# Optimization experiments

Hardware: AMD Instinct MI355X
Metric: run time of the kernel (lower is better)

The kernel has to match this reference:

```python
import jax, jax.numpy as jnp
import numpy as np

N_NODES = 100000
N_EDGES = 1600000
D_IN = 64
D_HID = 64
N_CLS = 4


def setup_inputs() -> dict:
    key = jax.random.key(0)
    ks = jax.random.split(key, 8)
    s = lambda d: 1.0 / np.sqrt(d)
    return {
        "node_features": jax.random.normal(ks[0], (N_NODES, D_IN), jnp.float32),
        "edge_src": jax.random.randint(ks[1], (N_EDGES,), 0, N_NODES, jnp.int32),
        "edge_dst": jax.random.randint(ks[2], (N_EDGES,), 0, N_NODES, jnp.int32),
        "W_self1": jax.random.normal(ks[3], (D_IN, D_HID), jnp.float32) * s(D_IN),
        "b_self1": jnp.zeros((D_HID,), jnp.float32),
        "W_neigh1": jax.random.normal(ks[4], (D_IN, D_HID), jnp.float32) * s(D_IN),
        "W_self2": jax.random.normal(ks[5], (D_HID, N_CLS), jnp.float32) * s(D_HID),
        "b_self2": jnp.zeros((N_CLS,), jnp.float32),
        "W_neigh2": jax.random.normal(ks[6], (D_HID, N_CLS), jnp.float32) * s(D_HID),
    }


def _sage_mean(h, edge_src, edge_dst, W_self, b_self, W_neigh, n_nodes):
    # mean aggregation over in-neighbors: gather src feats, segment-sum by dst
    msg_sum = jax.ops.segment_sum(h[edge_src], edge_dst, num_segments=n_nodes)
    deg = jax.ops.segment_sum(
        jnp.ones_like(edge_dst, dtype=h.dtype), edge_dst, num_segments=n_nodes
    )
    h_neigh = msg_sum / jnp.maximum(deg, 1.0)[:, None]
    # DGL SAGEConv: fc_self (with bias) + fc_neigh (no bias)
    return h @ W_self + b_self + h_neigh @ W_neigh


def reference(node_features, edge_src, edge_dst, W_self1, b_self1, W_neigh1,
              W_self2, b_self2, W_neigh2):
    n = node_features.shape[0]
    h1 = jnp.tanh(_sage_mean(node_features, edge_src, edge_dst,
                             W_self1, b_self1, W_neigh1, n))
    logits = _sage_mean(h1, edge_src, edge_dst, W_self2, b_self2, W_neigh2, n)
    return logits
```

## Files before the change

### kernel.cpp

```cpp
#include <hip/hip_runtime.h>
#include <hip/hip_bf16.h>
#include <stdint.h>

typedef unsigned char  u8;
typedef unsigned short u16;
typedef unsigned int   u32;
typedef __attribute__((ext_vector_type(8))) short bf16x8;
typedef __attribute__((ext_vector_type(2))) float f32x2;
typedef __attribute__((ext_vector_type(4))) float f32x4;
typedef __attribute__((ext_vector_type(4))) int   i32x4;
typedef __attribute__((ext_vector_type(2))) u32   u32x2;
typedef __attribute__((ext_vector_type(4))) u32   u32x4;

#define BKT_SHIFT 9
#define BKT_NODES 512
#define CAP 12288
#define BINBLK 512
#define KEYCAP 3200
#define GEMMBLK 512

__device__ __forceinline__ float bf2f(u16 u) { return __uint_as_float(((u32)u) << 16); }
__device__ __forceinline__ u16 f2bf(float f) {
    u32 u = __float_as_uint(f);
    u += 0x7FFFu + ((u >> 16) & 1u);
    return (u16)(u >> 16);
}
__device__ __forceinline__ int pkbf(float a, float b) {
    return (int)__builtin_amdgcn_perm(__float_as_uint(b), __float_as_uint(a), 0x07060302u);
}
__device__ __forceinline__ u8 f2fp8(float v) {
    int p = __builtin_amdgcn_cvt_pk_fp8_f32(v, v, 0, false);
    return (u8)(p & 0xff);
}


__global__ __launch_bounds__(256) void k_front(const float* __restrict__ X,
                                               const float* __restrict__ Ws,
                                               const float* __restrict__ b1,
                                               const float* __restrict__ Wn,
                                               u16* __restrict__ Zb,
                                               u8* __restrict__ Y,
                                               int n,
                                               const int* __restrict__ src,
                                               const int* __restrict__ dst,
                                               int* __restrict__ offT,
                                               u32* __restrict__ binned,
                                               int E, int chunk, int nb) {
    __shared__ __align__(16) char sm[17024];
    int t = threadIdx.x;

    if ((int)blockIdx.x < BINBLK) {
        u32* keys = (u32*)sm;
        int* h    = (int*)(sm + 12800);
        int* cur  = (int*)(sm + 13600);
        int* ws4  = (int*)(sm + 14400);
        int blk = blockIdx.x;
        int beg = blk * chunk, end = min(beg + chunk, E), m = max(0, end - beg);

        for (int i = t; i < nb; i += 256) h[i] = 0;
        __syncthreads();
        for (int i = beg + t; i < end; i += 256) atomicAdd(&h[dst[i] >> BKT_SHIFT], 1);
        __syncthreads();
        int v = (t < nb) ? h[t] : 0;
        int lane = t & 63, w = t >> 6;
        int incl = v;
#pragma unroll
        for (int o = 1; o < 64; o <<= 1) {
            int x = __shfl_up(incl, o, 64);
            if (lane >= o) incl += x;
        }
        if (lane == 63) ws4[w] = incl;
        __syncthreads();
        if (t == 0) {
            int run = 0;
#pragma unroll
            for (int i = 0; i < 4; i++) { ws4[4 + i] = run; run += ws4[i]; }
        }
        __syncthreads();
        int excl = incl - v + ws4[4 + w];
        int* orow = offT + (size_t)blk * (nb + 1);
        if (t < nb) { cur[t] = excl; orow[t] = excl; }
        if (t == nb - 1) orow[nb] = excl + v;
        __syncthreads();
        for (int i = beg + t; i < end; i += 256) {
            int d = dst[i], bk = d >> BKT_SHIFT;
            int p = atomicAdd(&cur[bk], 1);
            keys[p] = ((u32)src[i] << BKT_SHIFT) | (u32)(d & (BKT_NODES - 1));
        }
        __syncthreads();
        u32* outp = binned + (size_t)blk * chunk;
        for (int i = t; i < m; i += 256) outp[i] = keys[i];
        return;
    }

    u16* wl = (u16*)sm;
    for (int i = t; i < 8192; i += 256) {
        int k = i >> 7, c = i & 127;
        float wv = (c < 64) ? Ws[k * 64 + c] : Wn[k * 64 + (c - 64)];
        wl[k * 132 + c] = f2bf(wv);
    }
    __syncthreads();

    int wid = t >> 6, lane = t & 63;
    int lrow = lane & 15, lquad = lane >> 4;

    bf16x8 bfrag[8][2];
#pragma unroll
    for (int ct = 0; ct < 8; ct++)
#pragma unroll
        for (int kf = 0; kf < 2; kf++)
#pragma unroll
            for (int j = 0; j < 8; j++)
                bfrag[ct][kf][j] = (short)wl[(kf * 32 + lquad * 8 + j) * 132 + ct * 16 + lrow];

    float bias[4];
#pragma unroll
    for (int ct = 0; ct < 4; ct++) bias[ct] = b1[ct * 16 + lrow];

    int tiles = n >> 4;
    int tstride = GEMMBLK * 4;
    for (int tile = (blockIdx.x - BINBLK) * 4 + wid; tile < tiles; tile += tstride) {
        int nb4 = tile << 4;

        const float* xp = X + (size_t)(nb4 + lrow) * 64 + lquad * 8;
        f32x4 x0 = *(const f32x4*)(xp);
        f32x4 x1 = *(const f32x4*)(xp + 4);
        f32x4 x2 = *(const f32x4*)(xp + 32);
        f32x4 x3 = *(const f32x4*)(xp + 36);
        i32x4 p0, p1;
        p0.x = pkbf(x0.x, x0.y); p0.y = pkbf(x0.z, x0.w);
        p0.z = pkbf(x1.x, x1.y); p0.w = pkbf(x1.z, x1.w);
        p1.x = pkbf(x2.x, x2.y); p1.y = pkbf(x2.z, x2.w);
        p1.z = pkbf(x3.x, x3.y); p1.w = pkbf(x3.z, x3.w);
        bf16x8 af0 = __builtin_bit_cast(bf16x8, p0);
        bf16x8 af1 = __builtin_bit_cast(bf16x8, p1);

        f32x4 acc[8];
#pragma unroll
        for (int ct = 0; ct < 8; ct++) {
            f32x4 c = {0.f, 0.f, 0.f, 0.f};
            c = __builtin_amdgcn_mfma_f32_16x16x32_bf16(af0, bfrag[ct][0], c, 0, 0, 0);
            c = __builtin_amdgcn_mfma_f32_16x16x32_bf16(af1, bfrag[ct][1], c, 0, 0, 0);
            acc[ct] = c;
        }

        int rbase = nb4 + lquad * 4;
#pragma unroll
        for (int ct = 0; ct < 4; ct++)
#pragma unroll
            for (int r = 0; r < 4; r++)
                Zb[(size_t)(rbase + r) * 64 + ct * 16 + lrow] = f2bf(acc[ct][r] + bias[ct]);
#pragma unroll
        for (int ct = 0; ct < 4; ct++)
#pragma unroll
            for (int r = 0; r < 4; r++)
                Y[(size_t)(rbase + r) * 64 + ct * 16 + lrow] = f2fp8(acc[ct + 4][r]);
    }
}


__global__ __launch_bounds__(512) void k_csr(const u32* __restrict__ binned,
                                             const int* __restrict__ offT,
                                             int* __restrict__ rpb,
                                             int* __restrict__ rpe,
                                             int* __restrict__ col,
                                             int chunk, int nb, int n) {
    __shared__ __align__(16) u32 ed[CAP];
    __shared__ u32 srt[CAP];
    __shared__ int gst[BINBLK], gln[BINBLK], soff[BINBLK];
    __shared__ int cnt[BKT_NODES];
    __shared__ int wsum[8], woff[8];
    __shared__ int stot;
    int b = blockIdx.x, t = threadIdx.x;
    int lane = t & 63, w = t >> 6;

    {
        const int* row = offT + (size_t)t * (nb + 1);
        int s = row[b], e = row[b + 1];
        gst[t] = t * chunk + s;
        gln[t] = e - s;
    }
    __syncthreads();
    int v = gln[t];
    int incl = v;
#pragma unroll
    for (int o = 1; o < 64; o <<= 1) {
        int x = __shfl_up(incl, o, 64);
        if (lane >= o) incl += x;
    }
    if (lane == 63) wsum[w] = incl;
    __syncthreads();
    if (t == 0) {
        int run = 0;
#pragma unroll
        for (int i = 0; i < 8; i++) { woff[i] = run; run += wsum[i]; }
        stot = run;
    }
    __syncthreads();
    soff[t] = incl - v + woff[w];
    __syncthreads();
    int total = min(stot, CAP);
    for (int k = w; k < BINBLK; k += 8) {
        int g = gst[k], L = gln[k], o = soff[k];
        for (int i = lane; i < L && o + i < CAP; i += 64) ed[o + i] = binned[g + i];
    }
    cnt[t] = 0;
    __syncthreads();
    for (int i = t; i < total; i += 512)
        atomicAdd(&cnt[ed[i] & (BKT_NODES - 1)], 1);
    __syncthreads();
    int v2 = cnt[t];
    int incl2 = v2;
#pragma unroll
    for (int o = 1; o < 64; o <<= 1) {
        int x = __shfl_up(incl2, o, 64);
        if (lane >= o) incl2 += x;
    }
    if (lane == 63) wsum[w] = incl2;
    __syncthreads();
    if (t == 0) {
        int run = 0;
#pragma unroll
        for (int i = 0; i < 8; i++) { woff[i] = run; run += wsum[i]; }
    }
    __syncthreads();
    int excl2 = incl2 - v2 + woff[w];
    int gnode = b * BKT_NODES + t;
    int cb = b * CAP;
    if (gnode < n) { rpb[gnode] = cb + excl2; rpe[gnode] = cb + excl2 + v2; }
    cnt[t] = excl2;
    __syncthreads();
    for (int i = t; i < total; i += 512) {
        u32 e = ed[i];
        int p = atomicAdd(&cnt[e & (BKT_NODES - 1)], 1);
        srt[p] = e >> BKT_SHIFT;
    }
    __syncthreads();
    for (int i = t; i < total; i += 512) col[cb + i] = (int)srt[i];
}


__global__ __launch_bounds__(256) void k_gather1f(const int* __restrict__ rpb,
                                                  const int* __restrict__ rpe,
                                                  const int* __restrict__ col,
                                                  const u16* __restrict__ Zb,
                                                  const u8* __restrict__ Y,
                                                  const float* __restrict__ Ws2,
                                                  const float* __restrict__ b2,
                                                  const float* __restrict__ Wn2,
                                                  float* __restrict__ P,
                                                  u16* __restrict__ Q, int n) {
    __shared__ float wl[64 * 9];
    int t = threadIdx.x;
    for (int i = t; i < 512; i += 256) {
        int k = i >> 3, c = i & 7;
        float v = (c < 4) ? Ws2[k * 4 + c] : Wn2[k * 4 + (c - 4)];
        wl[((k & 7) * 8 + (k >> 3)) * 9 + c] = v;
    }
    float bb0 = b2[0], bb1 = b2[1], bb2 = b2[2], bb3 = b2[3];
    __syncthreads();

    int w = t >> 6;
    int g = (t >> 3) & 7;
    int l8 = t & 7;
    int node = blockIdx.x * 32 + w * 8 + g;
    if (node >= n) return;

    int beg = rpb[node], end = rpe[node];
    float a[8];
#pragma unroll
    for (int j = 0; j < 8; j++) a[j] = 0.f;

    const u8* yb = Y + (size_t)l8 * 8;
    int e = beg;
    for (; e + 4 <= end; e += 4) {
        i32x4 cv = *(const i32x4*)(col + e);
        u32x2 y0 = *(const u32x2*)(yb + (size_t)cv.x * 64);
        u32x2 y1 = *(const u32x2*)(yb + (size_t)cv.y * 64);
        u32x2 y2 = *(const u32x2*)(yb + (size_t)cv.z * 64);
        u32x2 y3 = *(const u32x2*)(yb + (size_t)cv.w * 64);
#pragma unroll
        for (int j = 0; j < 4; j++) {
            u32x2 yw = (j == 0) ? y0 : (j == 1) ? y1 : (j == 2) ? y2 : y3;
            f32x2 lo0 = __builtin_amdgcn_cvt_pk_f32_fp8(yw.x, false);
            f32x2 hi0 = __builtin_amdgcn_cvt_pk_f32_fp8(yw.x, true);
            f32x2 lo1 = __builtin_amdgcn_cvt_pk_f32_fp8(yw.y, false);
            f32x2 hi1 = __builtin_amdgcn_cvt_pk_f32_fp8(yw.y, true);
            a[0] += lo0.x; a[1] += lo0.y; a[2] += hi0.x; a[3] += hi0.y;
            a[4] += lo1.x; a[5] += lo1.y; a[6] += hi1.x; a[7] += hi1.y;
        }
    }
    for (; e < end; e++) {
        u32x2 yw = *(const u32x2*)(yb + (size_t)col[e] * 64);
        f32x2 lo0 = __builtin_amdgcn_cvt_pk_f32_fp8(yw.x, false);
        f32x2 hi0 = __builtin_amdgcn_cvt_pk_f32_fp8(yw.x, true);
        f32x2 lo1 = __builtin_amdgcn_cvt_pk_f32_fp8(yw.y, false);
        f32x2 hi1 = __builtin_amdgcn_cvt_pk_f32_fp8(yw.y, true);
        a[0] += lo0.x; a[1] += lo0.y; a[2] += hi0.x; a[3] += hi0.y;
        a[4] += lo1.x; a[5] += lo1.y; a[6] += hi1.x; a[7] += hi1.y;
    }

    float deg = (float)(end - beg);
    float inv = (deg > 0.f) ? 1.f / deg : 0.f;
    u32x4 zr = *(const u32x4*)(Zb + (size_t)node * 64 + l8 * 8);
    float h[8];
#pragma unroll
    for (int j = 0; j < 8; j++) {
        u32 word = (j < 2) ? zr.x : (j < 4) ? zr.y : (j < 6) ? zr.z : zr.w;
        u16 zv = (j & 1) ? (u16)(word >> 16) : (u16)(word & 0xffff);
        h[j] = tanhf(bf2f(zv) + a[j] * inv);
    }

    float r[8];
#pragma unroll
    for (int c = 0; c < 8; c++) r[c] = 0.f;
#pragma unroll
    for (int j = 0; j < 8; j++) {
        float hj = h[j];
        const float* wp = &wl[(j * 8 + l8) * 9];
#pragma unroll
        for (int c = 0; c < 8; c++) r[c] += hj * wp[c];
    }
#pragma unroll
    for (int m = 1; m < 8; m <<= 1)
#pragma unroll
        for (int c = 0; c < 8; c++) r[c] += __shfl_xor(r[c], m, 64);

    if (l8 == 0) {
        *(float4*)(P + (size_t)node * 4) =
            make_float4(r[0] + bb0, r[1] + bb1, r[2] + bb2, r[3] + bb3);
        ushort4 qv;
        qv.x = f2bf(r[4]); qv.y = f2bf(r[5]); qv.z = f2bf(r[6]); qv.w = f2bf(r[7]);
        *(ushort4*)(Q + (size_t)node * 4) = qv;
    }
}


__global__ __launch_bounds__(256) void k_gather2(const int* __restrict__ rpb,
                                                 const int* __restrict__ rpe,
                                                 const int* __restrict__ col,
                                                 const float* __restrict__ P,
                                                 const u16* __restrict__ Q,
                                                 float* __restrict__ out, int n) {
    int t = threadIdx.x;
    int g = t >> 3, l = t & 7;
    int node = blockIdx.x * 32 + g;
    if (node >= n) return;
    int beg = rpb[node], end = rpe[node];
    float a0 = 0.f, a1 = 0.f, a2 = 0.f, a3 = 0.f;
    for (int e = beg + l; e < end; e += 8) {
        ushort4 qv = *(const ushort4*)(Q + (size_t)col[e] * 4);
        a0 += bf2f(qv.x); a1 += bf2f(qv.y); a2 += bf2f(qv.z); a3 += bf2f(qv.w);
    }
#pragma unroll
    for (int m = 1; m < 8; m <<= 1) {
        a0 += __shfl_xor(a0, m, 64);
        a1 += __shfl_xor(a1, m, 64);
        a2 += __shfl_xor(a2, m, 64);
        a3 += __shfl_xor(a3, m, 64);
    }
    if (l == 0) {
        float deg = (float)(end - beg);
        float inv = (deg > 0.f) ? 1.f / deg : 0.f;
        float4 p = *(const float4*)(P + (size_t)node * 4);
        *(float4*)(out + (size_t)node * 4) =
            make_float4(p.x + a0 * inv, p.y + a1 * inv,
                        p.z + a2 * inv, p.w + a3 * inv);
    }
}


extern "C" void kernel_launch(void* const* d_in, const int* in_sizes, int n_in,
                              void* d_out, int out_size, void* d_ws, size_t ws_size,
                              hipStream_t stream) {
    const float* X   = (const float*)d_in[0];
    const int* esrc  = (const int*)d_in[1];
    const int* edst  = (const int*)d_in[2];
    const float* Ws1 = (const float*)d_in[3];
    const float* b1  = (const float*)d_in[4];
    const float* Wn1 = (const float*)d_in[5];
    const float* Ws2 = (const float*)d_in[6];
    const float* b2  = (const float*)d_in[7];
    const float* Wn2 = (const float*)d_in[8];
    float* out = (float*)d_out;

    const int n = in_sizes[0] / 64;
    const int E = in_sizes[1];
    const int nb = (n + BKT_NODES - 1) >> BKT_SHIFT;
    const int chunk = (E + BINBLK - 1) / BINBLK;

    size_t off = 0;
    char* base = (char*)d_ws;
    auto give = [&](size_t bytes) -> char* {
        char* p = base + off;
        off += (bytes + 255) & ~(size_t)255;
        return p;
    };
    int*   offT   = (int*)give((size_t)BINBLK * (nb + 1) * 4);
    int*   rpb    = (int*)give((size_t)n * 4);
    int*   rpe    = (int*)give((size_t)n * 4);
    u32*   binned = (u32*)give((size_t)BINBLK * chunk * 4);
    int*   col    = (int*)give((size_t)nb * CAP * 4);
    u16*   Zb     = (u16*)give((size_t)n * 64 * 2);
    u8*    Y      = (u8*)give((size_t)n * 64);
    float* P      = (float*)give((size_t)n * 4 * 4);
    u16*   Q      = (u16*)give((size_t)n * 4 * 2);

    k_front<<<BINBLK + GEMMBLK, 256, 0, stream>>>(
        X, Ws1, b1, Wn1, Zb, Y, n,
        esrc, edst, offT, binned, E, chunk, nb);

    k_csr<<<nb, 512, 0, stream>>>(binned, offT, rpb, rpe, col, chunk, nb, n);

    k_gather1f<<<(n + 31) / 32, 256, 0, stream>>>(rpb, rpe, col, Zb, Y,
                                                  Ws2, b2, Wn2, P, Q, n);
    k_gather2<<<(n + 31) / 32, 256, 0, stream>>>(rpb, rpe, col, P, Q, out, n);
}
```

Baseline: 176.5 us.

## Stage GEMM outputs in LDS for coalesced stores, unroll gather by 8, widen gather2 lanes

The front GEMM now writes its bf16 Z and fp8 Y tiles into per-wave padded shared-memory buffers and then stores them as 16-byte rows, replacing scattered 2-byte and 1-byte global stores. The layer-1 gather adds an 8-edge unrolled loop so more independent fp8 row loads are in flight per lane. The layer-2 gather uses 16 lanes per node instead of 8 and launches twice as many blocks. The larger shared allocation in the front kernel may reduce how many blocks fit per CU, and the wider gather may leave lanes idle on low-degree nodes.

```diff
diff --git a/kernel.cpp b/kernel.cpp
--- a/kernel.cpp
+++ b/kernel.cpp
@@ -16,7 +16,6 @@
 #define BKT_NODES 512
 #define CAP 12288
 #define BINBLK 512
-#define KEYCAP 3200
 #define GEMMBLK 512
 
 __device__ __forceinline__ float bf2f(u16 u) { return __uint_as_float(((u32)u) << 16); }
@@ -46,7 +45,7 @@
                                                int* __restrict__ offT,
                                                u32* __restrict__ binned,
                                                int E, int chunk, int nb) {
-    __shared__ __align__(16) char sm[17024];
+    __shared__ __align__(16) char sm[31744];
     int t = threadIdx.x;
 
     if ((int)blockIdx.x < BINBLK) {
@@ -116,6 +115,10 @@
     float bias[4];
 #pragma unroll
     for (int ct = 0; ct < 4; ct++) bias[ct] = b1[ct * 16 + lrow];
+
+    u16* Zs = (u16*)(sm + 16896 + wid * 3712);
+    u8*  Ys = (u8*)(sm + 16896 + wid * 3712 + 2432);
+    int srow = lane >> 2, sseg = lane & 3;
 
     int tiles = n >> 4;
     int tstride = GEMMBLK * 4;
@@ -144,17 +147,23 @@
             acc[ct] = c;
         }
 
-        int rbase = nb4 + lquad * 4;
 #pragma unroll
         for (int ct = 0; ct < 4; ct++)
 #pragma unroll
             for (int r = 0; r < 4; r++)
-                Zb[(size_t)(rbase + r) * 64 + ct * 16 + lrow] = f2bf(acc[ct][r] + bias[ct]);
+                Zs[(lquad * 4 + r) * 76 + ct * 16 + lrow] = f2bf(acc[ct][r] + bias[ct]);
 #pragma unroll
         for (int ct = 0; ct < 4; ct++)
 #pragma unroll
             for (int r = 0; r < 4; r++)
-                Y[(size_t)(rbase + r) * 64 + ct * 16 + lrow] = f2fp8(acc[ct + 4][r]);
+                Ys[(lquad * 4 + r) * 80 + ct * 16 + lrow] = f2fp8(acc[ct + 4][r]);
+
+        u32x4 z0 = *(const u32x4*)&Zs[srow * 76 + sseg * 16];
+        u32x4 z1 = *(const u32x4*)&Zs[srow * 76 + sseg * 16 + 8];
+        u32x4 yv = *(const u32x4*)&Ys[srow * 80 + sseg * 16];
+        *(u32x4*)(Zb + (size_t)(nb4 + srow) * 64 + sseg * 16) = z0;
+        *(u32x4*)(Zb + (size_t)(nb4 + srow) * 64 + sseg * 16 + 8) = z1;
+        *(u32x4*)(Y + (size_t)(nb4 + srow) * 64 + sseg * 16) = yv;
     }
 }
 
@@ -273,6 +282,29 @@
 
     const u8* yb = Y + (size_t)l8 * 8;
     int e = beg;
+    for (; e + 8 <= end; e += 8) {
+        i32x4 c0 = *(const i32x4*)(col + e);
+        i32x4 c1 = *(const i32x4*)(col + e + 4);
+        u32x2 y0 = *(const u32x2*)(yb + (size_t)c0.x * 64);
+        u32x2 y1 = *(const u32x2*)(yb + (size_t)c0.y * 64);
+        u32x2 y2 = *(const u32x2*)(yb + (size_t)c0.z * 64);
+        u32x2 y3 = *(const u32x2*)(yb + (size_t)c0.w * 64);
+        u32x2 y4 = *(const u32x2*)(yb + (size_t)c1.x * 64);
+        u32x2 y5 = *(const u32x2*)(yb + (size_t)c1.y * 64);
+        u32x2 y6 = *(const u32x2*)(yb + (size_t)c1.z * 64);
+        u32x2 y7 = *(const u32x2*)(yb + (size_t)c1.w * 64);
+#pragma unroll
+        for (int j = 0; j < 8; j++) {
+            u32x2 yw = (j == 0) ? y0 : (j == 1) ? y1 : (j == 2) ? y2 : (j == 3) ? y3
+                     : (j == 4) ? y4 : (j == 5) ? y5 : (j == 6) ? y6 : y7;
+            f32x2 lo0 = __builtin_amdgcn_cvt_pk_f32_fp8(yw.x, false);
+            f32x2 hi0 = __builtin_amdgcn_cvt_pk_f32_fp8(yw.x, true);
+            f32x2 lo1 = __builtin_amdgcn_cvt_pk_f32_fp8(yw.y, false);
+            f32x2 hi1 = __builtin_amdgcn_cvt_pk_f32_fp8(yw.y, true);
+            a[0] += lo0.x; a[1] += lo0.y; a[2] += hi0.x; a[3] += hi0.y;
+            a[4] += lo1.x; a[5] += lo1.y; a[6] += hi1.x; a[7] += hi1.y;
+        }
+    }
     for (; e + 4 <= end; e += 4) {
         i32x4 cv = *(const i32x4*)(col + e);
         u32x2 y0 = *(const u32x2*)(yb + (size_t)cv.x * 64);
@@ -343,17 +375,17 @@
                                                  const u16* __restrict__ Q,
                                                  float* __restrict__ out, int n) {
     int t = threadIdx.x;
-    int g = t >> 3, l = t & 7;
-    int node = blockIdx.x * 32 + g;
+    int g = t >> 4, l = t & 15;
+    int node = blockIdx.x * 16 + g;
     if (node >= n) return;
     int beg = rpb[node], end = rpe[node];
     float a0 = 0.f, a1 = 0.f, a2 = 0.f, a3 = 0.f;
-    for (int e = beg + l; e < end; e += 8) {
+    for (int e = beg + l; e < end; e += 16) {
         ushort4 qv = *(const ushort4*)(Q + (size_t)col[e] * 4);
         a0 += bf2f(qv.x); a1 += bf2f(qv.y); a2 += bf2f(qv.z); a3 += bf2f(qv.w);
     }
 #pragma unroll
-    for (int m = 1; m < 8; m <<= 1) {
+    for (int m = 1; m < 16; m <<= 1) {
         a0 += __shfl_xor(a0, m, 64);
         a1 += __shfl_xor(a1, m, 64);
         a2 += __shfl_xor(a2, m, 64);
@@ -414,5 +446,5 @@
 
     k_gather1f<<<(n + 31) / 32, 256, 0, stream>>>(rpb, rpe, col, Zb, Y,
                                                   Ws2, b2, Wn2, P, Q, n);
-    k_gather2<<<(n + 31) / 32, 256, 0, stream>>>(rpb, rpe, col, P, Q, out, n);
-}
+    k_gather2<<<(n + 15) / 16, 256, 0, stream>>>(rpb, rpe, col, P, Q, out, n);
+}
```

After: 177.3 us. About the same (+0.4%).
